# Kernel optimization log

Measured on AMD Instinct MI355X. Metric: run time of the kernel, lower is better.

Reference implementation:

```python
import jax, jax.numpy as jnp
import numpy as np

N, E, G = 50000, 800000, 512
D_NODE, D_EDGE, D_HID, D_OUT = 64, 16, 64, 1


def _lin(key, din, dout, bias=True):
    k1, k2 = jax.random.split(key)
    w = jax.random.normal(k1, (din, dout), jnp.float32) / np.sqrt(din)
    if bias:
        b = jax.random.normal(k2, (dout,), jnp.float32) * 0.01
        return w, b
    return w


def setup_inputs() -> dict:
    key = jax.random.key(0)
    ks = jax.random.split(key, 24)
    x = jax.random.normal(ks[0], (N, D_NODE), jnp.float32)
    edge_index = jax.random.randint(ks[1], (2, E), 0, N, jnp.int64)
    edge_attr = jax.random.normal(ks[2], (E, D_EDGE), jnp.float32)
    batch = jnp.sort(jax.random.randint(ks[3], (N,), 0, G, jnp.int64))
    wq1, bq1 = _lin(ks[4], D_NODE, D_HID)
    wk1, bk1 = _lin(ks[5], D_NODE, D_HID)
    wv1, bv1 = _lin(ks[6], D_NODE, D_HID)
    we1 = _lin(ks[7], D_EDGE, D_HID, bias=False)
    ws1, bs1 = _lin(ks[8], D_NODE, D_HID)
    wq2, bq2 = _lin(ks[9], D_HID, D_HID)
    wk2, bk2 = _lin(ks[10], D_HID, D_HID)
    wv2, bv2 = _lin(ks[11], D_HID, D_HID)
    we2 = _lin(ks[12], D_EDGE, D_HID, bias=False)
    ws2, bs2 = _lin(ks[13], D_HID, D_HID)
    w_fc1, b_fc1 = _lin(ks[14], D_HID, D_HID)
    w_fc2, b_fc2 = _lin(ks[15], D_HID, D_OUT)
    return dict(x=x, edge_index=edge_index, edge_attr=edge_attr, batch=batch,
                wq1=wq1, bq1=bq1, wk1=wk1, bk1=bk1, wv1=wv1, bv1=bv1, we1=we1, ws1=ws1, bs1=bs1,
                wq2=wq2, bq2=bq2, wk2=wk2, bk2=bk2, wv2=wv2, bv2=bv2, we2=we2, ws2=ws2, bs2=bs2,
                w_fc1=w_fc1, b_fc1=b_fc1, w_fc2=w_fc2, b_fc2=b_fc2)


def _leaky(z):
    return jnp.where(z >= 0, z, 0.01 * z)


def _transformer_conv(x, src, dst, e, wq, bq, wk, bk, wv, bv, we, ws, bs):
    # PyG TransformerConv, heads=1, concat=True, root_weight=True
    C = wq.shape[1]
    q = x @ wq + bq                      # [N,C]
    k = x @ wk + bk                      # [N,C]
    v = x @ wv + bv                      # [N,C]
    ee = e @ we                          # [E,C] (lin_edge, bias=False)
    ke = k[src] + ee                     # per-edge key
    ve = v[src] + ee                     # per-edge value
    score = jnp.sum(q[dst] * ke, axis=-1) / jnp.sqrt(jnp.float32(C))  # [E]
    m = jax.ops.segment_max(score, dst, num_segments=N)
    a = jnp.exp(score - m[dst])
    den = jax.ops.segment_sum(a, dst, num_segments=N)
    den = jnp.where(den == 0, 1.0, den)
    alpha = a / den[dst]
    agg = jax.ops.segment_sum(alpha[:, None] * ve, dst, num_segments=N)
    return agg + x @ ws + bs             # skip connection


def reference(x, edge_index, edge_attr, batch,
              wq1, bq1, wk1, bk1, wv1, bv1, we1, ws1, bs1,
              wq2, bq2, wk2, bk2, wv2, bv2, we2, ws2, bs2,
              w_fc1, b_fc1, w_fc2, b_fc2):
    src, dst = edge_index[0], edge_index[1]
    h = _leaky(_transformer_conv(x, src, dst, edge_attr, wq1, bq1, wk1, bk1, wv1, bv1, we1, ws1, bs1))
    atom_embs = _leaky(_transformer_conv(h, src, dst, edge_attr, wq2, bq2, wk2, bk2, wv2, bv2, we2, ws2, bs2))
    pooled = jax.ops.segment_sum(atom_embs, batch, num_segments=G)    # [G,C]
    norm = jnp.linalg.norm(pooled, axis=1, keepdims=True)
    h = pooled / jnp.maximum(norm, 1e-12)                             # F.normalize p=2
    h = _leaky(h @ w_fc1 + b_fc1)
    out = h @ w_fc2 + b_fc2
    return (out, atom_embs)
```

## Files before the change

### kernel.cpp

```cpp
#include <hip/hip_runtime.h>
#include <hip/hip_bf16.h>
#include <math.h>


typedef unsigned int uint32;
typedef unsigned short u16;
typedef __attribute__((ext_vector_type(8))) short short8;
typedef __attribute__((ext_vector_type(4))) float f32x4;

#define BW 256
#define CAP 5120
#define EPB 2048

__device__ __forceinline__ uint32 f2bf(float x) {
    uint32 u = __float_as_uint(x);
    u += 0x7fffu + ((u >> 16) & 1u);
    return u >> 16;
}
__device__ __forceinline__ float bf2f(u16 h) {
    return __uint_as_float(((uint32)h) << 16);
}


__global__ __launch_bounds__(256) void bucket_append(
    const int* __restrict__ dst, const int* __restrict__ src,
    int* __restrict__ bcount, uint2* __restrict__ buf, int E, int NB)
{
    __shared__ int hist[256], gbase[256], fill[256];
    int t = threadIdx.x;
    hist[t] = 0; fill[t] = 0;
    __syncthreads();
    int e0 = blockIdx.x * EPB;
    int d[8], s[8];
    #pragma unroll
    for (int k = 0; k < 8; ++k) {
        int e = e0 + k * 256 + t;
        if (e < E) {
            d[k] = dst[e]; s[k] = src[e];
            atomicAdd(&hist[d[k] >> 8], 1);
        } else d[k] = -1;
    }
    __syncthreads();
    if (t < NB && hist[t] > 0) gbase[t] = atomicAdd(&bcount[t], hist[t]);
    __syncthreads();
    #pragma unroll
    for (int k = 0; k < 8; ++k) {
        if (d[k] >= 0) {
            int e = e0 + k * 256 + t;
            int b = d[k] >> 8;
            int off = atomicAdd(&fill[b], 1);
            buf[(size_t)b * CAP + gbase[b] + off] =
                make_uint2(((uint32)(d[k] & 255) << 20) | (uint32)e, (uint32)s[k]);
        }
    }
}

__global__ __launch_bounds__(256) void csr_index(
    const int* __restrict__ bcount, const uint2* __restrict__ buf,
    int* __restrict__ row_ptr, int* __restrict__ gpos, int N, int E, int NB)
{
    __shared__ int sc[256], lh[256], lo[256], fill[256];
    int t = threadIdx.x;
    int b = blockIdx.x;
    sc[t] = (t < NB) ? bcount[t] : 0;
    lh[t] = 0; fill[t] = 0;
    __syncthreads();
    for (int off = 1; off < 256; off <<= 1) {
        int add = (t >= off) ? sc[t - off] : 0;
        __syncthreads();
        sc[t] += add;
        __syncthreads();
    }
    int cnt = bcount[b];
    int base = sc[b] - cnt;

    const uint2* bb = buf + (size_t)b * CAP;
    for (int i = t; i < cnt; i += 256) atomicAdd(&lh[(int)(bb[i].x >> 20)], 1);
    __syncthreads();
    int v = lh[t];
    lo[t] = v;
    __syncthreads();
    for (int off = 1; off < 256; off <<= 1) {
        int add = (t >= off) ? lo[t - off] : 0;
        __syncthreads();
        lo[t] += add;
        __syncthreads();
    }
    int ex = lo[t] - v;
    int d = b * BW + t;
    if (d < N) row_ptr[d] = base + ex;
    if (b == 0 && t == 0) row_ptr[N] = E;
    lo[t] = ex;
    __syncthreads();
    for (int i = t; i < cnt; i += 256) {
        int dl = (int)(bb[i].x >> 20);
        int off = atomicAdd(&fill[dl], 1);
        gpos[(size_t)b * CAP + i] = base + lo[dl] + off;
    }
}

__global__ __launch_bounds__(256) void csr_fill(
    const int* __restrict__ bcount, const uint2* __restrict__ buf,
    const int* __restrict__ gpos, const float* __restrict__ ea,
    int* __restrict__ csr_src, u16* __restrict__ ea16)
{
    int b = blockIdx.y;
    int slot = blockIdx.x * 256 + threadIdx.x;
    if (slot >= bcount[b]) return;
    size_t idx = (size_t)b * CAP + slot;
    uint2 ent = buf[idx];
    int gp = gpos[idx];
    csr_src[gp] = (int)ent.y;
    int e = (int)(ent.x & 0xFFFFFu);
    const float4* ev = (const float4*)(ea + (size_t)e * 16);
    float4 q0 = ev[0], q1 = ev[1], q2 = ev[2], q3 = ev[3];
    uint32* o = (uint32*)(ea16 + (size_t)gp * 16);
    o[0] = f2bf(q0.x) | (f2bf(q0.y) << 16);
    o[1] = f2bf(q0.z) | (f2bf(q0.w) << 16);
    o[2] = f2bf(q1.x) | (f2bf(q1.y) << 16);
    o[3] = f2bf(q1.z) | (f2bf(q1.w) << 16);
    o[4] = f2bf(q2.x) | (f2bf(q2.y) << 16);
    o[5] = f2bf(q2.z) | (f2bf(q2.w) << 16);
    o[6] = f2bf(q3.x) | (f2bf(q3.y) << 16);
    o[7] = f2bf(q3.z) | (f2bf(q3.w) << 16);
}


__global__ void wprep_kernel(
    const float* __restrict__ wq1, const float* __restrict__ bq1,
    const float* __restrict__ wk1, const float* __restrict__ wv1,
    const float* __restrict__ ws1, const float* __restrict__ we1,
    const float* __restrict__ wq2, const float* __restrict__ bq2,
    const float* __restrict__ wk2, const float* __restrict__ wv2,
    const float* __restrict__ ws2, const float* __restrict__ we2,
    u16* __restrict__ wt1, float* __restrict__ be1,
    u16* __restrict__ wt2, float* __restrict__ be2)
{
    int L = blockIdx.x;
    const float* wq = L ? wq2 : wq1;
    const float* bq = L ? bq2 : bq1;
    const float* wk = L ? wk2 : wk1;
    const float* wv = L ? wv2 : wv1;
    const float* ws = L ? ws2 : ws1;
    const float* we = L ? we2 : we1;
    u16* wt = L ? wt2 : wt1;
    float* be = L ? be2 : be1;
    int t = threadIdx.x;
    for (int i = t; i < 4096; i += 256) {
        int k = i >> 6, n = i & 63;
        wt[0 * 4096 + n * 64 + k] = (u16)f2bf(wq[k * 64 + n]);
        wt[1 * 4096 + n * 64 + k] = (u16)f2bf(wk[k * 64 + n]);
        wt[2 * 4096 + n * 64 + k] = (u16)f2bf(wv[k * 64 + n]);
        wt[3 * 4096 + n * 64 + k] = (u16)f2bf(ws[k * 64 + n]);
    }
    for (int i = t; i < 1024; i += 256) {
        int j = i >> 6, k = i & 63;
        float acc = 0.f;
        for (int c = 0; c < 64; ++c) acc = fmaf(wq[k * 64 + c], we[j * 64 + c], acc);
        wt[4 * 4096 + j * 64 + k] = (u16)f2bf(acc * 0.125f);
    }
    if (t < 16) {
        float acc = 0.f;
        for (int c = 0; c < 64; ++c) acc = fmaf(bq[c], we[t * 64 + c], acc);
        be[t] = acc * 0.125f;
    }
}


__global__ __launch_bounds__(256) void qkvs_mfma(
    const float* __restrict__ xin, const u16* __restrict__ wt,
    const float* __restrict__ bq, const float* __restrict__ bk,
    const float* __restrict__ bv, const float* __restrict__ bs,
    const float* __restrict__ be,
    float* __restrict__ qo, uint32* __restrict__ kvo,
    float* __restrict__ so, float* __restrict__ qeo, int N)
{
    int wave = threadIdx.x >> 6;
    int lane = threadIdx.x & 63;
    int quad = lane >> 4;
    int l16 = lane & 15;
    int n0 = blockIdx.x * 64 + wave * 16;
    int row = n0 + l16;
    int rn = (row < N) ? row : (N - 1);

    const float4* xr = (const float4*)(xin + (size_t)rn * 64);
    float4 u0 = xr[quad * 2 + 0], u1 = xr[quad * 2 + 1];
    float4 u2 = xr[8 + quad * 2 + 0], u3 = xr[8 + quad * 2 + 1];
    short8 a0, a1;
    a0[0] = (short)f2bf(u0.x); a0[1] = (short)f2bf(u0.y);
    a0[2] = (short)f2bf(u0.z); a0[3] = (short)f2bf(u0.w);
    a0[4] = (short)f2bf(u1.x); a0[5] = (short)f2bf(u1.y);
    a0[6] = (short)f2bf(u1.z); a0[7] = (short)f2bf(u1.w);
    a1[0] = (short)f2bf(u2.x); a1[1] = (short)f2bf(u2.y);
    a1[2] = (short)f2bf(u2.z); a1[3] = (short)f2bf(u2.w);
    a1[4] = (short)f2bf(u3.x); a1[5] = (short)f2bf(u3.y);
    a1[6] = (short)f2bf(u3.z); a1[7] = (short)f2bf(u3.w);

    const short8* w8 = (const short8*)wt;

    f32x4 acc[4][4];
    #pragma unroll
    for (int m = 0; m < 4; ++m)
        #pragma unroll
        for (int c = 0; c < 4; ++c) acc[m][c] = (f32x4){0.f, 0.f, 0.f, 0.f};
    f32x4 aqe = (f32x4){0.f, 0.f, 0.f, 0.f};

    #pragma unroll
    for (int m = 0; m < 4; ++m) {
        #pragma unroll
        for (int c = 0; c < 4; ++c) {
            short8 b0 = w8[m * 512 + (c * 16 + l16) * 8 + quad];
            short8 b1 = w8[m * 512 + (c * 16 + l16) * 8 + 4 + quad];
            acc[m][c] = __builtin_amdgcn_mfma_f32_16x16x32_bf16(a0, b0, acc[m][c], 0, 0, 0);
            acc[m][c] = __builtin_amdgcn_mfma_f32_16x16x32_bf16(a1, b1, acc[m][c], 0, 0, 0);
        }
    }
    {
        short8 b0 = w8[4 * 512 + l16 * 8 + quad];
        short8 b1 = w8[4 * 512 + l16 * 8 + 4 + quad];
        aqe = __builtin_amdgcn_mfma_f32_16x16x32_bf16(a0, b0, aqe, 0, 0, 0);
        aqe = __builtin_amdgcn_mfma_f32_16x16x32_bf16(a1, b1, aqe, 0, 0, 0);
    }

    int node0 = n0 + quad * 4;
    #pragma unroll
    for (int c = 0; c < 4; ++c) {
        int col = c * 16 + l16;
        float bQ = bq[col], bK = bk[col], bV = bv[col], bS = bs[col];
        #pragma unroll
        for (int r = 0; r < 4; ++r) {
            int node = node0 + r;
            if (node < N) {
                size_t off = (size_t)node * 64 + col;
                qo[off] = (acc[0][c][r] + bQ) * 0.125f;
                kvo[off] = f2bf(acc[1][c][r] + bK) | (f2bf(acc[2][c][r] + bV) << 16);
                so[off] = acc[3][c][r] + bS;
            }
        }
    }
    float beL = be[l16];
    #pragma unroll
    for (int r = 0; r < 4; ++r) {
        int node = node0 + r;
        if (node < N) qeo[(size_t)node * 16 + l16] = aqe[r] + beL;
    }
}


__global__ __launch_bounds__(256) void agg_kernel(
    const float* __restrict__ q, const uint32* __restrict__ kv,
    const float* __restrict__ qe, const float* __restrict__ we,
    const u16* __restrict__ ea16,
    const int* __restrict__ row_ptr, const int* __restrict__ csr_src,
    const float* __restrict__ skip_in, float* __restrict__ hout,
    const int* __restrict__ batch, float* __restrict__ pooled, int N)
{
    int lane = threadIdx.x & 63;
    int wid = (blockIdx.x << 2) + (threadIdx.x >> 6);
    if (wid >= N) return;
    int i = __builtin_amdgcn_readfirstlane(wid);

    int grp = lane >> 4;
    int pos = lane & 15;

    float4 qv = ((const float4*)(q + (size_t)i * 64))[pos];
    float qel = qe[(size_t)i * 16 + pos];
    float wer[16];
    #pragma unroll
    for (int j = 0; j < 16; ++j) wer[j] = we[j * 64 + lane];

    float den = 0.f, aj = 0.f;
    float o4x = 0.f, o4y = 0.f, o4z = 0.f, o4w = 0.f;

    int beg = row_ptr[i], end = row_ptr[i + 1];
    int last = end - 1;
    for (int p = beg; p < end; p += 16) {
        #pragma unroll
        for (int c = 0; c < 4; ++c) {
            int eg = p + 4 * c + grp;
            int si = (eg < end) ? eg : last;
            int s = csr_src[si];
            uint4 kb = ((const uint4*)(kv + (size_t)s * 64))[pos];
            float eav = bf2f(ea16[(size_t)(p + 4 * c) * 16 + lane]);
            float pa = eav * qel;
            pa = fmaf(qv.x, __uint_as_float(kb.x << 16), pa);
            pa = fmaf(qv.y, __uint_as_float(kb.y << 16), pa);
            pa = fmaf(qv.z, __uint_as_float(kb.z << 16), pa);
            pa = fmaf(qv.w, __uint_as_float(kb.w << 16), pa);
            pa += __shfl_xor(pa, 1);
            pa += __shfl_xor(pa, 2);
            pa += __shfl_xor(pa, 4);
            pa += __shfl_xor(pa, 8);
            float sc = (eg < end) ? pa : -1e30f;
            float w = __expf(sc);
            den += w;
            aj = fmaf(w, eav, aj);
            o4x = fmaf(w, __uint_as_float(kb.x & 0xffff0000u), o4x);
            o4y = fmaf(w, __uint_as_float(kb.y & 0xffff0000u), o4y);
            o4z = fmaf(w, __uint_as_float(kb.z & 0xffff0000u), o4z);
            o4w = fmaf(w, __uint_as_float(kb.w & 0xffff0000u), o4w);
        }
    }

    o4x += __shfl_xor(o4x, 16); o4x += __shfl_xor(o4x, 32);
    o4y += __shfl_xor(o4y, 16); o4y += __shfl_xor(o4y, 32);
    o4z += __shfl_xor(o4z, 16); o4z += __shfl_xor(o4z, 32);
    o4w += __shfl_xor(o4w, 16); o4w += __shfl_xor(o4w, 32);
    aj  += __shfl_xor(aj, 16);  aj  += __shfl_xor(aj, 32);
    den += __shfl_xor(den, 16); den += __shfl_xor(den, 32);

    int srcl = lane >> 2;
    float t0 = __shfl(o4x, srcl), t1 = __shfl(o4y, srcl);
    float t2 = __shfl(o4z, srcl), t3 = __shfl(o4w, srcl);
    int r2 = lane & 3;
    float o = (r2 == 0) ? t0 : (r2 == 1) ? t1 : (r2 == 2) ? t2 : t3;

    #pragma unroll
    for (int j = 0; j < 16; ++j) o = fmaf(__shfl(aj, j), wer[j], o);

    float dinv = (den > 0.f) ? 1.f / den : 0.f;
    float r = fmaf(o, dinv, skip_in[(size_t)i * 64 + lane]);
    r = (r >= 0.f) ? r : 0.01f * r;
    hout[(size_t)i * 64 + lane] = r;
    if (pooled) atomicAdd(&pooled[(size_t)batch[i] * 64 + lane], r);
}


__global__ void head_kernel(const float* __restrict__ pooled,
                            const float* __restrict__ w1, const float* __restrict__ b1,
                            const float* __restrict__ w2, const float* __restrict__ b2,
                            float* __restrict__ out, int G) {
    int g = blockIdx.x;
    int lane = threadIdx.x;
    __shared__ float hl[64];
    float p = pooled[g * 64 + lane];
    float ss = p * p;
    #pragma unroll
    for (int off = 32; off; off >>= 1) ss += __shfl_xor(ss, off);
    float hn = p / fmaxf(sqrtf(ss), 1e-12f);
    hl[lane] = hn;
    __syncthreads();
    float acc = b1[lane];
    #pragma unroll
    for (int j = 0; j < 64; ++j) acc = fmaf(hl[j], w1[j * 64 + lane], acc);
    acc = (acc >= 0.f) ? acc : 0.01f * acc;
    float r = acc * w2[lane];
    #pragma unroll
    for (int off = 32; off; off >>= 1) r += __shfl_xor(r, off);
    if (lane == 0) out[g] = r + b2[0];
}


extern "C" void kernel_launch(void* const* d_in, const int* in_sizes, int n_in,
                              void* d_out, int out_size, void* d_ws, size_t ws_size,
                              hipStream_t stream) {
    const float* x     = (const float*)d_in[0];
    const int*   ei    = (const int*)  d_in[1];
    const float* ea    = (const float*)d_in[2];
    const int*   batch = (const int*)  d_in[3];
    const float *wq1=(const float*)d_in[4],  *bq1=(const float*)d_in[5];
    const float *wk1=(const float*)d_in[6],  *bk1=(const float*)d_in[7];
    const float *wv1=(const float*)d_in[8],  *bv1=(const float*)d_in[9];
    const float *we1=(const float*)d_in[10];
    const float *ws1=(const float*)d_in[11], *bs1=(const float*)d_in[12];
    const float *wq2=(const float*)d_in[13], *bq2=(const float*)d_in[14];
    const float *wk2=(const float*)d_in[15], *bk2=(const float*)d_in[16];
    const float *wv2=(const float*)d_in[17], *bv2=(const float*)d_in[18];
    const float *we2=(const float*)d_in[19];
    const float *ws2=(const float*)d_in[20], *bs2=(const float*)d_in[21];
    const float *wf1=(const float*)d_in[22], *bf1=(const float*)d_in[23];
    const float *wf2=(const float*)d_in[24], *bf2=(const float*)d_in[25];

    int N = in_sizes[0] / 64;
    int E = in_sizes[2] / 16;
    int G = out_size - N * 64;
    int NB = (N + BW - 1) / BW;

    const int* srcA = ei;
    const int* dstA = ei + E;

    char* w = (char*)d_ws;
    float*  qb      = (float*)w;  w += (size_t)N * 64 * 4;
    uint32* kvb     = (uint32*)w; w += (size_t)N * 64 * 4;
    float*  hb      = (float*)w;  w += (size_t)N * 64 * 4;
    float*  qeb     = (float*)w;  w += (size_t)N * 16 * 4;
    float*  pooled  = (float*)w;  w += (size_t)G * 64 * 4;
    int* bcount     = (int*)w;    w += 256 * 4;
    int* row_ptr    = (int*)w;    w += (size_t)(N + 1) * 4;
    u16* wt1        = (u16*)w;    w += (4 * 4096 + 1024) * 2;
    u16* wt2        = (u16*)w;    w += (4 * 4096 + 1024) * 2;
    float* be1      = (float*)w;  w += 16 * 4;
    float* be2      = (float*)w;  w += 16 * 4;
    int* csr_src    = (int*)w;    w += (size_t)E * 4;
    u16* ea16       = (u16*)w;    w += ((size_t)E * 16 + 1024) * 2;
    uint2* bbuf     = (uint2*)w;  w += (size_t)NB * CAP * 8;
    int* gpos       = (int*)w;    w += (size_t)NB * CAP * 4;

    hipMemsetAsync(pooled, 0, (size_t)G * 64 * 4 + 256 * 4, stream);

    wprep_kernel<<<2, 256, 0, stream>>>(wq1, bq1, wk1, wv1, ws1, we1,
                                        wq2, bq2, wk2, wv2, ws2, we2,
                                        wt1, be1, wt2, be2);
    bucket_append<<<(E + EPB - 1) / EPB, 256, 0, stream>>>(dstA, srcA, bcount, bbuf, E, NB);
    csr_index<<<NB, 256, 0, stream>>>(bcount, bbuf, row_ptr, gpos, N, E, NB);
    csr_fill<<<dim3(CAP / 256, NB), 256, 0, stream>>>(bcount, bbuf, gpos, ea,
                                                      csr_src, ea16);

    float* outp = (float*)d_out;
    float* atom = outp + G;

    int qBlocks = (N + 63) / 64;
    int aggBlocks = (N + 3) / 4;

    qkvs_mfma<<<qBlocks, 256, 0, stream>>>(x, wt1, bq1, bk1, bv1, bs1, be1,
                                           qb, kvb, hb, qeb, N);
    agg_kernel<<<aggBlocks, 256, 0, stream>>>(qb, kvb, qeb, we1, ea16, row_ptr, csr_src,
                                              hb, hb, nullptr, nullptr, N);

    qkvs_mfma<<<qBlocks, 256, 0, stream>>>(hb, wt2, bq2, bk2, bv2, bs2, be2,
                                           qb, kvb, atom, qeb, N);
    agg_kernel<<<aggBlocks, 256, 0, stream>>>(qb, kvb, qeb, we2, ea16, row_ptr, csr_src,
                                              atom, atom, batch, pooled, N);

    head_kernel<<<G, 64, 0, stream>>>(pooled, wf1, bf1, wf2, bf2, outp, G);
}
```

Baseline: 381.0 us.

## Drop csr_fill; stage CSR (src, edge id) in LDS and gather edge attrs by id

```diff
diff --git a/kernel.cpp b/kernel.cpp
--- a/kernel.cpp
+++ b/kernel.cpp
@@ -57,9 +57,10 @@
 
 __global__ __launch_bounds__(256) void csr_index(
     const int* __restrict__ bcount, const uint2* __restrict__ buf,
-    int* __restrict__ row_ptr, int* __restrict__ gpos, int N, int E, int NB)
+    int* __restrict__ row_ptr, uint2* __restrict__ csr_se, int N, int E, int NB)
 {
     __shared__ int sc[256], lh[256], lo[256], fill[256];
+    __shared__ uint2 se[CAP];
     int t = threadIdx.x;
     int b = blockIdx.x;
     sc[t] = (t < NB) ? bcount[t] : 0;
@@ -93,28 +94,22 @@
     lo[t] = ex;
     __syncthreads();
     for (int i = t; i < cnt; i += 256) {
-        int dl = (int)(bb[i].x >> 20);
+        uint2 ent = bb[i];
+        int dl = (int)(ent.x >> 20);
         int off = atomicAdd(&fill[dl], 1);
-        gpos[(size_t)b * CAP + i] = base + lo[dl] + off;
-    }
-}
-
-__global__ __launch_bounds__(256) void csr_fill(
-    const int* __restrict__ bcount, const uint2* __restrict__ buf,
-    const int* __restrict__ gpos, const float* __restrict__ ea,
-    int* __restrict__ csr_src, u16* __restrict__ ea16)
-{
-    int b = blockIdx.y;
-    int slot = blockIdx.x * 256 + threadIdx.x;
-    if (slot >= bcount[b]) return;
-    size_t idx = (size_t)b * CAP + slot;
-    uint2 ent = buf[idx];
-    int gp = gpos[idx];
-    csr_src[gp] = (int)ent.y;
-    int e = (int)(ent.x & 0xFFFFFu);
+        se[lo[dl] + off] = make_uint2(ent.y, ent.x & 0xFFFFFu);
+    }
+    __syncthreads();
+    for (int i = t; i < cnt; i += 256) csr_se[base + i] = se[i];
+}
+
+__global__ __launch_bounds__(256) void ea16cvt(const float* __restrict__ ea,
+                                               u16* __restrict__ ea16e, int E) {
+    int e = blockIdx.x * blockDim.x + threadIdx.x;
+    if (e >= E) return;
     const float4* ev = (const float4*)(ea + (size_t)e * 16);
     float4 q0 = ev[0], q1 = ev[1], q2 = ev[2], q3 = ev[3];
-    uint32* o = (uint32*)(ea16 + (size_t)gp * 16);
+    uint32* o = (uint32*)(ea16e + (size_t)e * 16);
     o[0] = f2bf(q0.x) | (f2bf(q0.y) << 16);
     o[1] = f2bf(q0.z) | (f2bf(q0.w) << 16);
     o[2] = f2bf(q1.x) | (f2bf(q1.y) << 16);
@@ -250,8 +245,8 @@
 __global__ __launch_bounds__(256) void agg_kernel(
     const float* __restrict__ q, const uint32* __restrict__ kv,
     const float* __restrict__ qe, const float* __restrict__ we,
-    const u16* __restrict__ ea16,
-    const int* __restrict__ row_ptr, const int* __restrict__ csr_src,
+    const u16* __restrict__ ea16e,
+    const int* __restrict__ row_ptr, const uint2* __restrict__ csr_se,
     const float* __restrict__ skip_in, float* __restrict__ hout,
     const int* __restrict__ batch, float* __restrict__ pooled, int N)
 {
@@ -279,9 +274,9 @@
         for (int c = 0; c < 4; ++c) {
             int eg = p + 4 * c + grp;
             int si = (eg < end) ? eg : last;
-            int s = csr_src[si];
-            uint4 kb = ((const uint4*)(kv + (size_t)s * 64))[pos];
-            float eav = bf2f(ea16[(size_t)(p + 4 * c) * 16 + lane]);
+            uint2 se = csr_se[si];
+            uint4 kb = ((const uint4*)(kv + (size_t)se.x * 64))[pos];
+            float eav = bf2f(ea16e[(size_t)se.y * 16 + pos]);
             float pa = eav * qel;
             pa = fmaf(qv.x, __uint_as_float(kb.x << 16), pa);
             pa = fmaf(qv.y, __uint_as_float(kb.y << 16), pa);
@@ -391,10 +386,9 @@
     u16* wt2        = (u16*)w;    w += (4 * 4096 + 1024) * 2;
     float* be1      = (float*)w;  w += 16 * 4;
     float* be2      = (float*)w;  w += 16 * 4;
-    int* csr_src    = (int*)w;    w += (size_t)E * 4;
-    u16* ea16       = (u16*)w;    w += ((size_t)E * 16 + 1024) * 2;
+    uint2* csr_se   = (uint2*)w;  w += (size_t)E * 8;
+    u16* ea16e      = (u16*)w;    w += ((size_t)E * 16 + 1024) * 2;
     uint2* bbuf     = (uint2*)w;  w += (size_t)NB * CAP * 8;
-    int* gpos       = (int*)w;    w += (size_t)NB * CAP * 4;
 
     hipMemsetAsync(pooled, 0, (size_t)G * 64 * 4 + 256 * 4, stream);
 
@@ -402,9 +396,8 @@
                                         wq2, bq2, wk2, wv2, ws2, we2,
                                         wt1, be1, wt2, be2);
     bucket_append<<<(E + EPB - 1) / EPB, 256, 0, stream>>>(dstA, srcA, bcount, bbuf, E, NB);
-    csr_index<<<NB, 256, 0, stream>>>(bcount, bbuf, row_ptr, gpos, N, E, NB);
-    csr_fill<<<dim3(CAP / 256, NB), 256, 0, stream>>>(bcount, bbuf, gpos, ea,
-                                                      csr_src, ea16);
+    ea16cvt<<<(E + 255) / 256, 256, 0, stream>>>(ea, ea16e, E);
+    csr_index<<<NB, 256, 0, stream>>>(bcount, bbuf, row_ptr, csr_se, N, E, NB);
 
     float* outp = (float*)d_out;
     float* atom = outp + G;
@@ -414,12 +407,12 @@
 
     qkvs_mfma<<<qBlocks, 256, 0, stream>>>(x, wt1, bq1, bk1, bv1, bs1, be1,
                                            qb, kvb, hb, qeb, N);
-    agg_kernel<<<aggBlocks, 256, 0, stream>>>(qb, kvb, qeb, we1, ea16, row_ptr, csr_src,
+    agg_kernel<<<aggBlocks, 256, 0, stream>>>(qb, kvb, qeb, we1, ea16e, row_ptr, csr_se,
                                               hb, hb, nullptr, nullptr, N);
 
     qkvs_mfma<<<qBlocks, 256, 0, stream>>>(hb, wt2, bq2, bk2, bv2, bs2, be2,
                                            qb, kvb, atom, qeb, N);
-    agg_kernel<<<aggBlocks, 256, 0, stream>>>(qb, kvb, qeb, we2, ea16, row_ptr, csr_src,
+    agg_kernel<<<aggBlocks, 256, 0, stream>>>(qb, kvb, qeb, we2, ea16e, row_ptr, csr_se,
                                               atom, atom, batch, pooled, N);
 
     head_kernel<<<G, 64, 0, stream>>>(pooled, wf1, bf1, wf2, bf2, outp, G);
```

New measurement: 361.8 us. -5.0%, faster.
